# Kernel tuning notes

Measured on AMD Instinct MI355X. Metric: run time of the kernel, lower is better.

The kernel has to match this reference:

```python
import jax, jax.numpy as jnp
import numpy as np
import math

EMBED_DIM = 2048
NUM_HEADS = 32
GROUPS = 4
HEAD_DIM = EMBED_DIM // NUM_HEADS  # 64
HPG = NUM_HEADS // GROUPS          # heads per group = 8


def setup_inputs() -> dict:
    key = jax.random.key(0)
    k_x, k_wq, k_bq, k_wkv, k_bkv = jax.random.split(key, 5)
    B, L = 4, 4096
    scale = 1.0 / math.sqrt(EMBED_DIM)
    return {
        "x": jax.random.normal(k_x, (B, L, EMBED_DIM), dtype=jnp.float32),
        "Wq": jax.random.normal(k_wq, (EMBED_DIM, EMBED_DIM), dtype=jnp.float32) * scale,
        "bq": jax.random.normal(k_bq, (EMBED_DIM,), dtype=jnp.float32) * 0.01,
        "Wkv": jax.random.normal(k_wkv, (EMBED_DIM, 2 * HEAD_DIM * GROUPS), dtype=jnp.float32) * scale,
        "bkv": jax.random.normal(k_bkv, (2 * HEAD_DIM * GROUPS,), dtype=jnp.float32) * 0.01,
    }


def reference(x, Wq, bq, Wkv, bkv):
    B, L, _ = x.shape
    # projections
    q = (x @ Wq + bq).reshape(B, L, GROUPS, HPG, HEAD_DIM)          # blghd
    kv = (x @ Wkv + bkv).reshape(B, L, GROUPS, 2, HEAD_DIM)
    k, v = kv[:, :, :, 0], kv[:, :, :, 1]                            # blgd
    # scores: q @ k^T with k of shape (..., 1, head_dim) -> (..., HPG, 1)
    scores = jnp.einsum("blghd,blgd->blgh", q, k)[..., None] / math.sqrt(HEAD_DIM)
    attn = jax.nn.softmax(scores, axis=-1)                           # size-1 axis -> ones
    # attn @ v: (..., HPG, 1) @ (..., 1, head_dim) -> (..., HPG, head_dim)
    out = attn * v[:, :, :, None, :]                                 # blghd
    return out.reshape(B, L, EMBED_DIM)
```

## Files before the change

kernel.cpp:

```cpp
#include <hip/hip_runtime.h>


#define EMBED 2048
#define BM 32
#define BK 32
#define KITERS (EMBED / BK)
#define BUFH (256 * BK)
#define VS 260

typedef _Float16 half8 __attribute__((ext_vector_type(8)));
typedef float f32x4 __attribute__((ext_vector_type(4)));

#define ASM_BARRIER() asm volatile("s_waitcnt lgkmcnt(0)\ns_barrier" ::: "memory")

__global__ __launch_bounds__(256) void prep_b(const float* __restrict__ Wkv,
                                              _Float16* __restrict__ Bt) {
  const int t = threadIdx.x;
  const int kb = blockIdx.x * 8;
  const int vcol = ((t >> 6) * 128) + 64 + (t & 63);
  float v[8];
#pragma unroll
  for (int i = 0; i < 8; ++i) v[i] = Wkv[(size_t)(kb + i) * 512 + vcol];
  half8 h;
#pragma unroll
  for (int i = 0; i < 8; ++i) h[i] = (_Float16)v[i];
  *(half8*)&Bt[(size_t)t * EMBED + kb] = h;
}

__device__ __forceinline__ half8 cvt8(f32x4 lo, f32x4 hi) {
  half8 r;
#pragma unroll
  for (int j = 0; j < 4; ++j) {
    r[j] = (_Float16)lo[j];
    r[4 + j] = (_Float16)hi[j];
  }
  return r;
}

__global__ __launch_bounds__(256, 3) void gqa_main(
    const float* __restrict__ x, const _Float16* __restrict__ Bt,
    const float* __restrict__ bkv, float* __restrict__ out) {
  __shared__ __align__(16) char smem[BM * VS * 4];
  _Float16* Bs0 = (_Float16*)smem;
  _Float16* Bs1 = Bs0 + BUFH;
  float* Vs = (float*)smem;

  const int tid = threadIdx.x;
  const int wave = tid >> 6;
  const int lane = tid & 63;
  const int lm = lane & 15;
  const int lq = lane >> 4;
  const int r0 = blockIdx.x * BM;

  const int srow = tid >> 2, sc = tid & 3;
  const _Float16* bgp = Bt + (size_t)srow * EMBED + sc * 8;
  int bofs[4];
#pragma unroll
  for (int p = 0; p < 4; ++p)
    bofs[p] = (srow + p * 64) * BK + ((sc ^ (srow & 3)) * 8);

  int bro[4];
#pragma unroll
  for (int ni = 0; ni < 4; ++ni) {
    const int row = wave * 64 + ni * 16 + lm;
    bro[ni] = row * BK + ((lq ^ (row & 3)) * 8);
  }

  const float* ag = x + (size_t)(r0 + lm) * EMBED + lq * 8;

  half8 bA[4], bB[4];
  f32x4 aA[2][2], aB[2][2];
  f32x4 acc[2][4] = {};

#define LOADB(kt, R)                                                     \
  {                                                                      \
    const _Float16* p_ = bgp + (kt) * BK;                                \
    _Pragma("unroll") for (int i_ = 0; i_ < 4; ++i_)                     \
        R[i_] = *(const half8*)(p_ + (size_t)i_ * 64 * EMBED);           \
  }
#define LOADA(kt, R)                                                     \
  {                                                                      \
    _Pragma("unroll") for (int mi_ = 0; mi_ < 2; ++mi_) {                \
      const float* p_ = ag + (size_t)mi_ * 16 * EMBED + (kt) * BK;       \
      R[mi_][0] = *(const f32x4*)p_;                                     \
      R[mi_][1] = *(const f32x4*)(p_ + 4);                               \
    }                                                                    \
  }
#define STOREB(R, base)                                                  \
  {                                                                      \
    _Pragma("unroll") for (int i_ = 0; i_ < 4; ++i_)                     \
        *(half8*)((base) + bofs[i_]) = R[i_];                            \
  }
#define MFMA8(base, af0, af1)                                            \
  {                                                                      \
    _Pragma("unroll") for (int ni_ = 0; ni_ < 4; ++ni_) {                \
      half8 bf_ = *(const half8*)((base) + bro[ni_]);                    \
      acc[0][ni_] = __builtin_amdgcn_mfma_f32_16x16x32_f16(              \
          af0, bf_, acc[0][ni_], 0, 0, 0);                               \
      acc[1][ni_] = __builtin_amdgcn_mfma_f32_16x16x32_f16(              \
          af1, bf_, acc[1][ni_], 0, 0, 0);                               \
    }                                                                    \
  }

  LOADB(0, bA);
  LOADB(1, bB);
  LOADA(0, aA);
  LOADA(1, aB);
  STOREB(bA, Bs0);
  ASM_BARRIER();

  for (int kt = 0; kt < KITERS; kt += 2) {
    STOREB(bB, Bs1);
    {
      half8 af0 = cvt8(aA[0][0], aA[0][1]);
      half8 af1 = cvt8(aA[1][0], aA[1][1]);
      if (kt + 2 < KITERS) {
        LOADB(kt + 2, bA);
        LOADA(kt + 2, aA);
      }
      MFMA8(Bs0, af0, af1);
    }
    ASM_BARRIER();

    if (kt + 2 < KITERS) STOREB(bA, Bs0);
    {
      half8 af0 = cvt8(aB[0][0], aB[0][1]);
      half8 af1 = cvt8(aB[1][0], aB[1][1]);
      if (kt + 3 < KITERS) {
        LOADB(kt + 3, bB);
        LOADA(kt + 3, aB);
      }
      MFMA8(Bs1, af0, af1);
    }
    ASM_BARRIER();
  }

#pragma unroll
  for (int ni = 0; ni < 4; ++ni) {
    const int ncol = wave * 64 + ni * 16 + lm;
    const float bias = bkv[((ncol >> 6) * 128) + 64 + (ncol & 63)];
#pragma unroll
    for (int mi = 0; mi < 2; ++mi) {
      f32x4 v = acc[mi][ni];
#pragma unroll
      for (int r = 0; r < 4; ++r) {
        Vs[(mi * 16 + lq * 4 + r) * VS + ncol] = v[r] + bias;
      }
    }
  }
  __syncthreads();

  f32x4* out4 = (f32x4*)out;
  const size_t obase = (size_t)r0 * 512;
#pragma unroll 4
  for (int i = 0; i < 64; ++i) {
    const int f = i * 256 + tid;
    const int m = f >> 9;
    const int c4 = f & 511;
    const int g = c4 >> 7;
    const int d4 = c4 & 15;
    out4[obase + (size_t)f] = *(const f32x4*)&Vs[m * VS + g * 64 + d4 * 4];
  }
}

extern "C" void kernel_launch(void* const* d_in, const int* in_sizes, int n_in,
                              void* d_out, int out_size, void* d_ws, size_t ws_size,
                              hipStream_t stream) {
  const float* x = (const float*)d_in[0];
  const float* Wkv = (const float*)d_in[3];
  const float* bkv = (const float*)d_in[4];
  float* out = (float*)d_out;
  _Float16* Bt = (_Float16*)d_ws;

  prep_b<<<256, 256, 0, stream>>>(Wkv, Bt);
  gqa_main<<<(4 * 4096) / BM, 256, 0, stream>>>(x, Bt, bkv, out);
}
```

Measured before the change: 319.7 us.

## Replace LDS-staged B tiles with direct per-wave global fragment loads

Restructures the V-projection GEMM so each wave computes a 16x64 tile, loading A and B fragments straight from global memory into registers instead of staging B through shared memory with barriers. The grid now splits the 4 groups across blocks (64 rows x 64 cols per block), shrinking LDS to a small per-wave output staging buffer and raising the occupancy hint. This drops LDS stores and block barriers in the main loop. The cost is that each x row tile is read by 4 blocks instead of once, which may raise L2/HBM traffic, and B fragments are refetched per wave.

```diff
diff --git a/kernel.cpp b/kernel.cpp
--- a/kernel.cpp
+++ b/kernel.cpp
@@ -2,16 +2,10 @@
 
 
 #define EMBED 2048
-#define BM 32
-#define BK 32
-#define KITERS (EMBED / BK)
-#define BUFH (256 * BK)
-#define VS 260
+#define KITERS 64
 
 typedef _Float16 half8 __attribute__((ext_vector_type(8)));
 typedef float f32x4 __attribute__((ext_vector_type(4)));
-
-#define ASM_BARRIER() asm volatile("s_waitcnt lgkmcnt(0)\ns_barrier" ::: "memory")
 
 __global__ __launch_bounds__(256) void prep_b(const float* __restrict__ Wkv,
                                               _Float16* __restrict__ Bt) {
@@ -37,129 +31,90 @@
   return r;
 }
 
-__global__ __launch_bounds__(256, 3) void gqa_main(
+__global__ __launch_bounds__(256, 4) void gqa_main(
     const float* __restrict__ x, const _Float16* __restrict__ Bt,
     const float* __restrict__ bkv, float* __restrict__ out) {
-  __shared__ __align__(16) char smem[BM * VS * 4];
-  _Float16* Bs0 = (_Float16*)smem;
-  _Float16* Bs1 = Bs0 + BUFH;
-  float* Vs = (float*)smem;
+  __shared__ float Vs[4 * 16 * 68];
 
   const int tid = threadIdx.x;
   const int wave = tid >> 6;
   const int lane = tid & 63;
   const int lm = lane & 15;
   const int lq = lane >> 4;
-  const int r0 = blockIdx.x * BM;
 
-  const int srow = tid >> 2, sc = tid & 3;
-  const _Float16* bgp = Bt + (size_t)srow * EMBED + sc * 8;
-  int bofs[4];
-#pragma unroll
-  for (int p = 0; p < 4; ++p)
-    bofs[p] = (srow + p * 64) * BK + ((sc ^ (srow & 3)) * 8);
+  const int nb = blockIdx.x & 3;
+  const int mb = blockIdx.x >> 2;
+  const int m0 = mb * 64 + wave * 16;
 
-  int bro[4];
-#pragma unroll
-  for (int ni = 0; ni < 4; ++ni) {
-    const int row = wave * 64 + ni * 16 + lm;
-    bro[ni] = row * BK + ((lq ^ (row & 3)) * 8);
+  const float* ag = x + (size_t)(m0 + lm) * EMBED + lq * 8;
+  const _Float16* bg = Bt + (size_t)(nb * 64 + lm) * EMBED + lq * 8;
+
+  f32x4 acc[4] = {};
+  f32x4 aA[2], aB[2];
+  half8 bA[4], bB[4];
+
+#define LOADA(kt, R)                              \
+  {                                               \
+    const float* p_ = ag + (kt) * 32;             \
+    R[0] = *(const f32x4*)p_;                     \
+    R[1] = *(const f32x4*)(p_ + 4);               \
+  }
+#define LOADB(kt, R)                                                        \
+  {                                                                         \
+    const _Float16* p_ = bg + (kt) * 32;                                    \
+    _Pragma("unroll") for (int ni_ = 0; ni_ < 4; ++ni_)                     \
+        R[ni_] = *(const half8*)(p_ + (size_t)ni_ * 16 * EMBED);            \
+  }
+#define MFMA4(af, R)                                                          \
+  {                                                                          \
+    _Pragma("unroll") for (int ni_ = 0; ni_ < 4; ++ni_)                      \
+        acc[ni_] = __builtin_amdgcn_mfma_f32_16x16x32_f16(af, R[ni_],        \
+                                                          acc[ni_], 0, 0, 0); \
   }
 
-  const float* ag = x + (size_t)(r0 + lm) * EMBED + lq * 8;
-
-  half8 bA[4], bB[4];
-  f32x4 aA[2][2], aB[2][2];
-  f32x4 acc[2][4] = {};
-
-#define LOADB(kt, R)                                                     \
-  {                                                                      \
-    const _Float16* p_ = bgp + (kt) * BK;                                \
-    _Pragma("unroll") for (int i_ = 0; i_ < 4; ++i_)                     \
-        R[i_] = *(const half8*)(p_ + (size_t)i_ * 64 * EMBED);           \
-  }
-#define LOADA(kt, R)                                                     \
-  {                                                                      \
-    _Pragma("unroll") for (int mi_ = 0; mi_ < 2; ++mi_) {                \
-      const float* p_ = ag + (size_t)mi_ * 16 * EMBED + (kt) * BK;       \
-      R[mi_][0] = *(const f32x4*)p_;                                     \
-      R[mi_][1] = *(const f32x4*)(p_ + 4);                               \
-    }                                                                    \
-  }
-#define STOREB(R, base)                                                  \
-  {                                                                      \
-    _Pragma("unroll") for (int i_ = 0; i_ < 4; ++i_)                     \
-        *(half8*)((base) + bofs[i_]) = R[i_];                            \
-  }
-#define MFMA8(base, af0, af1)                                            \
-  {                                                                      \
-    _Pragma("unroll") for (int ni_ = 0; ni_ < 4; ++ni_) {                \
-      half8 bf_ = *(const half8*)((base) + bro[ni_]);                    \
-      acc[0][ni_] = __builtin_amdgcn_mfma_f32_16x16x32_f16(              \
-          af0, bf_, acc[0][ni_], 0, 0, 0);                               \
-      acc[1][ni_] = __builtin_amdgcn_mfma_f32_16x16x32_f16(              \
-          af1, bf_, acc[1][ni_], 0, 0, 0);                               \
-    }                                                                    \
-  }
-
+  LOADA(0, aA);
   LOADB(0, bA);
+  LOADA(1, aB);
   LOADB(1, bB);
-  LOADA(0, aA);
-  LOADA(1, aB);
-  STOREB(bA, Bs0);
-  ASM_BARRIER();
 
   for (int kt = 0; kt < KITERS; kt += 2) {
-    STOREB(bB, Bs1);
     {
-      half8 af0 = cvt8(aA[0][0], aA[0][1]);
-      half8 af1 = cvt8(aA[1][0], aA[1][1]);
+      half8 af = cvt8(aA[0], aA[1]);
+      MFMA4(af, bA);
       if (kt + 2 < KITERS) {
+        LOADA(kt + 2, aA);
         LOADB(kt + 2, bA);
-        LOADA(kt + 2, aA);
       }
-      MFMA8(Bs0, af0, af1);
     }
-    ASM_BARRIER();
-
-    if (kt + 2 < KITERS) STOREB(bA, Bs0);
     {
-      half8 af0 = cvt8(aB[0][0], aB[0][1]);
-      half8 af1 = cvt8(aB[1][0], aB[1][1]);
+      half8 af = cvt8(aB[0], aB[1]);
+      MFMA4(af, bB);
       if (kt + 3 < KITERS) {
+        LOADA(kt + 3, aB);
         LOADB(kt + 3, bB);
-        LOADA(kt + 3, aB);
-      }
-      MFMA8(Bs1, af0, af1);
-    }
-    ASM_BARRIER();
-  }
-
-#pragma unroll
-  for (int ni = 0; ni < 4; ++ni) {
-    const int ncol = wave * 64 + ni * 16 + lm;
-    const float bias = bkv[((ncol >> 6) * 128) + 64 + (ncol & 63)];
-#pragma unroll
-    for (int mi = 0; mi < 2; ++mi) {
-      f32x4 v = acc[mi][ni];
-#pragma unroll
-      for (int r = 0; r < 4; ++r) {
-        Vs[(mi * 16 + lq * 4 + r) * VS + ncol] = v[r] + bias;
       }
     }
   }
-  __syncthreads();
 
-  f32x4* out4 = (f32x4*)out;
-  const size_t obase = (size_t)r0 * 512;
-#pragma unroll 4
-  for (int i = 0; i < 64; ++i) {
-    const int f = i * 256 + tid;
-    const int m = f >> 9;
-    const int c4 = f & 511;
-    const int g = c4 >> 7;
+  float* vw = Vs + wave * (16 * 68);
+#pragma unroll
+  for (int ni = 0; ni < 4; ++ni) {
+    const float bias = bkv[nb * 128 + 64 + ni * 16 + lm];
+#pragma unroll
+    for (int r = 0; r < 4; ++r) {
+      vw[(lq * 4 + r) * 68 + ni * 16 + lm] = acc[ni][r] + bias;
+    }
+  }
+  asm volatile("s_waitcnt lgkmcnt(0)" ::: "memory");
+
+  f32x4* out4 = (f32x4*)(out + (size_t)m0 * EMBED + nb * 512);
+#pragma unroll 8
+  for (int i = 0; i < 32; ++i) {
+    const int f = i * 64 + lane;
+    const int row = f >> 7;
+    const int c4 = f & 127;
     const int d4 = c4 & 15;
-    out4[obase + (size_t)f] = *(const f32x4*)&Vs[m * VS + g * 64 + d4 * 4];
+    out4[(size_t)row * 512 + c4] = *(const f32x4*)&vw[row * 68 + d4 * 4];
   }
 }
 
@@ -173,5 +128,5 @@
   _Float16* Bt = (_Float16*)d_ws;
 
   prep_b<<<256, 256, 0, stream>>>(Wkv, Bt);
-  gqa_main<<<(4 * 4096) / BM, 256, 0, stream>>>(x, Bt, bkv, out);
+  gqa_main<<<256 * 4, 256, 0, stream>>>(x, Bt, bkv, out);
 }
```

After: 376.8 us. 1.18x slower.
